# Kernel optimization log

Hardware: AMD Instinct MI355X
Metric: run time of the kernel (lower is better)

## Reference

```python
import jax, jax.numpy as jnp
import numpy as np

B, T = 128, 64
EMB, ACT = 1536, 12
STOCH, DETER, HIDDEN, ENS = 32, 1024, 1024, 5
MIN_STD = 0.1
UPDATE_BIAS = -1.0


def _ln(x, scale, bias, eps=1e-5):
    m = jnp.mean(x, -1, keepdims=True)
    v = jnp.mean((x - m) ** 2, -1, keepdims=True)
    return (x - m) * jax.lax.rsqrt(v + eps) * scale + bias


def setup_inputs():
    key = jax.random.key(0)
    ks = jax.random.split(key, 10)
    w = lambda k, s, sc=0.02: jax.random.normal(k, s, jnp.float32) * sc
    return dict(
        embed=jax.random.normal(ks[0], (B, T, EMB), jnp.float32),
        action=jax.random.normal(ks[1], (B, T, ACT), jnp.float32),
        is_first=(jax.random.uniform(ks[2], (B, T)) < 0.05),
        ens_index=jax.random.randint(ks[3], (T,), 0, ENS),
        W_img_in=w(ks[4], (STOCH + ACT, HIDDEN)), b_img_in=jnp.zeros((HIDDEN,)),
        g_img_in=jnp.ones((HIDDEN,)), bn_img_in=jnp.zeros((HIDDEN,)),
        W_gru=w(ks[5], (HIDDEN + DETER, 3 * DETER)), b_gru=jnp.zeros((3 * DETER,)),
        g_gru=jnp.ones((3 * DETER,)), bn_gru=jnp.zeros((3 * DETER,)),
        W_img_out=w(ks[6], (ENS, DETER, HIDDEN)), b_img_out=jnp.zeros((ENS, HIDDEN)),
        g_img_out=jnp.ones((ENS, HIDDEN)), bn_img_out=jnp.zeros((ENS, HIDDEN)),
        W_img_dist=w(ks[7], (ENS, HIDDEN, 2 * STOCH)), b_img_dist=jnp.zeros((ENS, 2 * STOCH)),
        W_obs_out=w(ks[8], (DETER + EMB, HIDDEN)), b_obs_out=jnp.zeros((HIDDEN,)),
        g_obs_out=jnp.ones((HIDDEN,)), bn_obs_out=jnp.zeros((HIDDEN,)),
        W_obs_dist=w(ks[9], (HIDDEN, 2 * STOCH)), b_obs_dist=jnp.zeros((2 * STOCH,)),
    )


def _observe(embed, action, is_first, ens_index,
             W_img_in, b_img_in, g_img_in, bn_img_in,
             W_gru, b_gru, g_gru, bn_gru,
             W_img_out, b_img_out, g_img_out, bn_img_out,
             W_img_dist, b_img_dist,
             W_obs_out, b_obs_out, g_obs_out, bn_obs_out,
             W_obs_dist, b_obs_dist):
    def step(carry, xs):
        stoch, deter = carry
        a, e, first, idx = xs  # [B,ACT], [B,EMB], [B], []
        m = (1.0 - first.astype(jnp.float32))[:, None]  # is_first resets prev state/action
        a, stoch, deter = a * m, stoch * m, deter * m
        # img_step: input MLP -> GRU cell (norm=True, update_bias=-1, Tanh)
        x = jax.nn.elu(_ln(jnp.concatenate([stoch, a], -1) @ W_img_in + b_img_in, g_img_in, bn_img_in))
        parts = _ln(jnp.concatenate([x, deter], -1) @ W_gru + b_gru, g_gru, bn_gru)
        reset, cand, update = jnp.split(parts, 3, -1)
        reset = jax.nn.sigmoid(reset)
        cand = jnp.tanh(reset * cand)
        update = jax.nn.sigmoid(update + UPDATE_BIAS)
        deter = update * cand + (1.0 - update) * deter
        # ensemble sufficient stats (all heads computed, one selected, as original)
        hs = jax.nn.elu(_ln(jnp.einsum('bd,kdh->kbh', deter, W_img_out) + b_img_out[:, None, :],
                            g_img_out[:, None, :], bn_img_out[:, None, :]))
        ds = jnp.einsum('kbh,khs->kbs', hs, W_img_dist) + b_img_dist[:, None, :]
        pmean, pstd = jnp.split(ds[idx], 2, -1)
        pstd = jax.nn.softplus(pstd) + MIN_STD
        prior_stoch = pmean  # deterministic mode of Normal
        # obs_step posterior
        xo = jax.nn.elu(_ln(jnp.concatenate([deter, e], -1) @ W_obs_out + b_obs_out, g_obs_out, bn_obs_out))
        omean, ostd = jnp.split(xo @ W_obs_dist + b_obs_dist, 2, -1)
        ostd = jax.nn.softplus(ostd) + MIN_STD
        post_stoch = omean
        out = jnp.concatenate([omean, ostd, post_stoch, pmean, pstd, prior_stoch, deter], -1)
        return (post_stoch, deter), out

    init = (jnp.zeros((B, STOCH), jnp.float32), jnp.zeros((B, DETER), jnp.float32))
    xs = (jnp.swapaxes(action, 0, 1), jnp.swapaxes(embed, 0, 1),
          jnp.swapaxes(is_first, 0, 1), ens_index)
    _, ys = jax.lax.scan(step, init, xs)  # [T, B, 6*STOCH + DETER]
    return jnp.swapaxes(ys, 0, 1)  # [B, T, 6*STOCH + DETER]


def reference(embed, action, is_first, ens_index,
              W_img_in, b_img_in, g_img_in, bn_img_in,
              W_gru, b_gru, g_gru, bn_gru,
              W_img_out, b_img_out, g_img_out, bn_img_out,
              W_img_dist, b_img_dist,
              W_obs_out, b_obs_out, g_obs_out, bn_obs_out,
              W_obs_dist, b_obs_dist):
    return _observe(embed, action, is_first, ens_index,
                    W_img_in, b_img_in, g_img_in, bn_img_in,
                    W_gru, b_gru, g_gru, bn_gru,
                    W_img_out, b_img_out, g_img_out, bn_img_out,
                    W_img_dist, b_img_dist,
                    W_obs_out, b_obs_out, g_obs_out, bn_obs_out,
                    W_obs_dist, b_obs_dist)
```

## Files before the change

kernel.cpp:

```cpp
#include <hip/hip_runtime.h>
#include <hip/hip_bf16.h>
#include <math.h>

using bf16 = __hip_bfloat16;
using short8 = __attribute__((ext_vector_type(8))) short;
using f32x4  = __attribute__((ext_vector_type(4))) float;

#define B_     128
#define T_     64
#define EMB_   1536
#define ACT_   12
#define STOCH_ 32
#define DETER_ 1024
#define HID_   1024
#define GRUN_  3072
#define GRUK_  2048
#define OBSK_  2560
#define OUTW_  1216

#define PW1   0
#define Pb1   45056
#define Pg1   46080
#define Pbn1  47104
#define Pbg   48128
#define Pgg   51200
#define Pbng  54272
#define Pb3   57344
#define Pg3   62464
#define Pbn3  67584
#define Pb4   72704
#define Pb5   73024
#define Pg5   74048
#define Pbn5  75072
#define Pb6   76096
#define PW4   76160
#define PW6   403840
#define PTOT  469376

__device__ inline float bf2f(bf16 v){ return __bfloat162float(v); }
__device__ inline bf16  f2bf(float v){ return __float2bfloat16(v); }
__device__ inline float elu_(float x){ return x > 0.f ? x : expm1f(x); }
__device__ inline float sigm_(float x){ return 1.f/(1.f+expf(-x)); }
__device__ inline float softplus_(float x){ return fmaxf(x,0.f) + log1pf(expf(-fabsf(x))); }
__device__ inline void stout(void* out, int dt, size_t i, float v){
  if(dt) ((bf16*)out)[i] = f2bf(v); else ((float*)out)[i] = v;
}
__device__ inline float maskv(const void* isf, int enc, int idx){
  float fv;
  if(enc==0)      fv = (float)((const int*)isf)[idx];
  else if(enc==1) fv = (float)((const unsigned char*)isf)[idx];
  else if(enc==2) fv = bf2f(((const bf16*)isf)[idx]);
  else            fv = ((const float*)isf)[idx];
  return (fv != 0.f) ? 0.f : 1.f;
}

__device__ inline void block_reduce2w(float& a, float& b, float* sm, int nw){
  __syncthreads();
  for(int off=32; off>0; off>>=1){
    a += __shfl_down(a, off);
    b += __shfl_down(b, off);
  }
  int w = threadIdx.x >> 6;
  if((threadIdx.x & 63) == 0){ sm[2*w] = a; sm[2*w+1] = b; }
  __syncthreads();
  float sa = 0.f, sb = 0.f;
  for(int i=0;i<nw;i++){ sa += sm[2*i]; sb += sm[2*i+1]; }
  a = sa; b = sb;
}

__global__ void k_detect(const unsigned short* emb, const unsigned char* isf, int* dflag){
  __shared__ int c0, c1, c2;
  if(threadIdx.x==0){ c0=0; c1=0; c2=0; }
  __syncthreads();
  if(blockIdx.x == 0){
    int c = 0;
    for(int i=threadIdx.x; i<2048; i+=256){
      unsigned short u = emb[2*i];
      int exp8 = (u >> 7) & 0xFF;
      if(exp8 > 140) c++;
    }
    atomicAdd(&c0, c);
    __syncthreads();
    if(threadIdx.x==0) dflag[0] = (c0 < 100) ? 1 : 0;
  } else {
    for(int i=threadIdx.x; i<B_*T_; i+=256){
      unsigned char c = isf[i];
      if(c == 0x3F){
        if((i & 3) == 1) atomicOr(&c0, 1);
        else if((i & 3) == 3) atomicOr(&c1, 1);
      }
      if(c == 1 && (i & 3) != 0) atomicOr(&c2, 1);
    }
    __syncthreads();
    if(threadIdx.x==0)
      dflag[1] = c0 ? 2 : (c1 ? 3 : (c2 ? 1 : 0));
  }
}

struct PDesc { const void* src[17]; int cum[18]; };
#define SEG0 1834
#define SEG1 12288
#define SEG2 96
#define SEG3 1536
#define SEG4 1280
#define SEG5 640

__device__ void transpose_dev(const void* src, bf16* dst, int K, int N,
                              int tk, int tn, int head, int dt,
                              unsigned short (*t)[72]){
  size_t hoff = (size_t)head * K * N;
  unsigned short* d = (unsigned short*)dst + hoff;
  int tx = threadIdx.x & 63, ty0 = threadIdx.x >> 6;
  int k0 = tk*64, n0 = tn*64;
  #pragma unroll
  for(int i=0;i<16;i++){
    int ty = ty0*16+i;
    size_t off = hoff + (size_t)(k0+ty)*N + n0+tx;
    unsigned short v;
    if(dt) v = ((const unsigned short*)src)[off];
    else { bf16 b = f2bf(((const float*)src)[off]); v = *(unsigned short*)&b; }
    t[ty][tx] = v;
  }
  __syncthreads();
  #pragma unroll
  for(int i=0;i<16;i++){ int ty = ty0*16+i; d[(size_t)(n0+ty)*K + k0+tx] = t[tx][ty]; }
}

__global__ __launch_bounds__(256) void k_setup(
    PDesc pd, float* paramF, const int* dflag,
    const void* embed, bf16* embB, const void* action, float* actF,
    const void* w8, bf16* WgT, const void* w12, bf16* W3T,
    const void* w18, bf16* W5T)
{
  __shared__ unsigned short ts[64][72];
  int bid = blockIdx.x, tid = threadIdx.x;
  int dt = dflag[0];
  if(bid < SEG0){
    int g = bid*256 + tid;
    if(g >= PTOT) return;
    int s = 0;
    while(g >= pd.cum[s+1]) s++;
    int off = g - pd.cum[s];
    paramF[g] = dt ? bf2f(((const bf16*)pd.src[s])[off]) : ((const float*)pd.src[s])[off];
    return;
  }
  bid -= SEG0;
  if(bid < SEG1){
    int i0 = (bid*256 + tid)*4;
    #pragma unroll
    for(int k=0;k<4;k++){
      int i = i0+k;
      embB[i] = dt ? ((const bf16*)embed)[i] : f2bf(((const float*)embed)[i]);
    }
    return;
  }
  bid -= SEG1;
  if(bid < SEG2){
    int i0 = (bid*256 + tid)*4;
    int n = B_*T_*ACT_;
    #pragma unroll
    for(int k=0;k<4;k++){
      int i = i0+k;
      if(i < n) actF[i] = dt ? bf2f(((const bf16*)action)[i]) : ((const float*)action)[i];
    }
    return;
  }
  bid -= SEG2;
  if(bid < SEG3){
    transpose_dev(w8, WgT, GRUK_, GRUN_, bid/48, bid%48, 0, dt, ts);
    return;
  }
  bid -= SEG3;
  if(bid < SEG4){
    int head = bid/256, rem = bid%256;
    transpose_dev(w12, W3T, DETER_, HID_, rem/16, rem%16, head, dt, ts);
    return;
  }
  bid -= SEG4;
  transpose_dev(w18, W5T, OBSK_, HID_, bid/16, bid%16, 0, dt, ts);
}

__global__ __launch_bounds__(256) void k_gemm(
    int mode, int t,
    const bf16* A2, const bf16* deterB, const bf16* embB,
    const bf16* WgT, const bf16* W3T, const bf16* W5T,
    float* z2p, float* z3p, float* z5p, const int* ens_index)
{
  __shared__ float red[8192];
  int bid = blockIdx.x;
  const bf16 *A0 = nullptr, *A1 = nullptr, *BT; float* Cdst;
  int N, ldb, s0 = 0, s1 = 0, split = 1<<30, k0, kc;
  if(mode == 0){
    if(bid < 192){
      int ct = bid % 96, part = bid / 96;
      N = GRUN_; ldb = GRUK_; BT = WgT + (size_t)ct*32*GRUK_;
      A0 = A2; s0 = GRUK_;
      k0 = part*1024; kc = 1024;
      Cdst = z2p + (size_t)part*B_*GRUN_ + ct*32;
    } else {
      int b2 = bid - 192;
      int ct = b2 & 31, part = b2 >> 5;
      N = HID_; ldb = OBSK_; BT = W5T + (size_t)ct*32*OBSK_;
      split = DETER_;
      A1 = embB + (size_t)t*EMB_; s1 = T_*EMB_;
      k0 = 1024 + part*768; kc = 768;
      Cdst = z5p + (size_t)(2+part)*B_*HID_ + ct*32;
    }
  } else if(bid < 64){
    int ct = bid & 31, part = bid >> 5;
    int idx = ens_index[t];
    N = HID_; ldb = DETER_; BT = W3T + (size_t)idx*DETER_*HID_ + (size_t)ct*32*DETER_;
    A0 = deterB; s0 = DETER_;
    k0 = part*512; kc = 512;
    Cdst = z3p + (size_t)part*B_*HID_ + ct*32;
  } else {
    int b2 = bid - 64;
    int ct = b2 & 31, part = b2 >> 5;
    N = HID_; ldb = OBSK_; BT = W5T + (size_t)ct*32*OBSK_;
    A0 = deterB; s0 = DETER_;
    k0 = part*512; kc = 512;
    Cdst = z5p + (size_t)part*B_*HID_ + ct*32;
  }
  int tid = threadIdx.x;
  int wave = tid >> 6, lane = tid & 63;
  int quad = lane >> 4, lo = lane & 15;
  int kw0 = k0 + wave*(kc>>2), kw1 = kw0 + (kc>>2);
  f32x4 acc[8][2];
  #pragma unroll
  for(int rf=0;rf<8;rf++){ acc[rf][0]=(f32x4)0.f; acc[rf][1]=(f32x4)0.f; }
  for(int kk=kw0; kk<kw1; kk+=32){
    int kf = kk + quad*8;
    const bf16* Ab; int str, ko;
    if(kf < split){ Ab=A0; str=s0; ko=kf; } else { Ab=A1; str=s1; ko=kf-split; }
    short8 af[8], bfg[2];
    #pragma unroll
    for(int rf=0;rf<8;rf++)
      af[rf] = *(const short8*)(const void*)(Ab + (size_t)(16*rf+lo)*str + ko);
    #pragma unroll
    for(int c=0;c<2;c++)
      bfg[c] = *(const short8*)(const void*)(BT + (size_t)(16*c+lo)*ldb + kf);
    #pragma unroll
    for(int rf=0;rf<8;rf++){
      acc[rf][0] = __builtin_amdgcn_mfma_f32_16x16x32_bf16(af[rf], bfg[0], acc[rf][0], 0,0,0);
      acc[rf][1] = __builtin_amdgcn_mfma_f32_16x16x32_bf16(af[rf], bfg[1], acc[rf][1], 0,0,0);
    }
  }
  if(wave >= 2){
    #pragma unroll
    for(int rf=0;rf<8;rf++)
      #pragma unroll
      for(int c=0;c<2;c++)
        *(f32x4*)&red[(((wave-2)*16) + rf*2 + c)*256 + lane*4] = acc[rf][c];
  }
  __syncthreads();
  if(wave < 2){
    #pragma unroll
    for(int rf=0;rf<8;rf++)
      #pragma unroll
      for(int c=0;c<2;c++)
        acc[rf][c] += *(const f32x4*)&red[((wave*16) + rf*2 + c)*256 + lane*4];
  }
  __syncthreads();
  if(wave < 2){
    #pragma unroll
    for(int rf=0;rf<8;rf++)
      #pragma unroll
      for(int c=0;c<2;c++)
        *(f32x4*)&red[((wave*16) + rf*2 + c)*256 + lane*4] = acc[rf][c];
  }
  __syncthreads();
  #pragma unroll
  for(int i=0;i<4;i++){
    int r = (tid>>3) + 32*i;
    int col0 = (tid&7)*4;
    int rf = r>>4, rr = r&15, q = rr>>2, g = rr&3;
    f32x4 v;
    #pragma unroll
    for(int j=0;j<4;j++){
      int col = col0+j; int c = col>>4, lo2 = col&15;
      int lane2 = q*16+lo2;
      v[j] = red[(rf*2 + c)*256 + lane2*4 + g]
           + red[(16 + rf*2 + c)*256 + lane2*4 + g];
    }
    *(f32x4*)(Cdst + (size_t)r*N + col0) = v;
  }
}

__global__ __launch_bounds__(1024) void k_gru(
    const float* z2p, const float* paramF, const int* dflag,
    const float* determ, float* deter, bf16* deterB, void* out, int t)
{
  __shared__ float sm[32];
  int b = blockIdx.x, tid = threadIdx.x;
  int dt = dflag[0];
  float zz[3]; float s=0.f, s2=0.f;
  #pragma unroll
  for(int i=0;i<3;i++){
    int h = tid + 1024*i;
    float acc = paramF[Pbg + h]
              + z2p[(size_t)b*GRUN_ + h]
              + z2p[(size_t)(B_ + b)*GRUN_ + h];
    zz[i]=acc; s+=acc; s2+=acc*acc;
  }
  block_reduce2w(s, s2, sm, 16);
  float mean = s/GRUN_, var = s2/GRUN_ - mean*mean;
  float rstd = rsqrtf(fmaxf(var,0.f) + 1e-5f);
  {
    float lnr = (zz[0] - mean)*rstd*paramF[Pgg+tid     ] + paramF[Pbng+tid     ];
    float lnc = (zz[1] - mean)*rstd*paramF[Pgg+tid+1024] + paramF[Pbng+tid+1024];
    float lnu = (zz[2] - mean)*rstd*paramF[Pgg+tid+2048] + paramF[Pbng+tid+2048];
    float reset = sigm_(lnr);
    float cand  = tanhf(reset*lnc);
    float upd   = sigm_(lnu - 1.f);
    float dn = upd*cand + (1.f-upd)*determ[b*DETER_+tid];
    deter[b*DETER_+tid]  = dn;
    deterB[b*DETER_+tid] = f2bf(dn);
    stout(out, dt, ((size_t)b*T_+t)*OUTW_ + 192 + tid, dn);
  }
}

__global__ __launch_bounds__(1024) void k_tail(
    const float* z3p, const float* z5p, const float* paramF, const int* dflag,
    const float* actF, const void* isf,
    const float* deter, float* determ, bf16* A2,
    void* out, const int* ens_index, int t)
{
  __shared__ float hs[1024], xo[1024];
  __shared__ float red[1024];
  __shared__ float dsO[128];
  __shared__ float in44[48];
  __shared__ float sm[32];
  int b = blockIdx.x, tid = threadIdx.x;
  int dt = dflag[0];
  int idx = ens_index[t];
  float a3 = z3p[(size_t)b*HID_ + tid] + z3p[(size_t)(B_ + b)*HID_ + tid]
           + paramF[Pb3 + idx*HID_ + tid];
  float a5 = z5p[(size_t)b*HID_ + tid] + z5p[(size_t)(B_ + b)*HID_ + tid]
           + z5p[(size_t)(2*B_ + b)*HID_ + tid] + z5p[(size_t)(3*B_ + b)*HID_ + tid]
           + paramF[Pb5 + tid];
  float s3=a3, q3=a3*a3, s5=a5, q5=a5*a5;
  block_reduce2w(s3, q3, sm, 16);
  block_reduce2w(s5, q5, sm, 16);
  float m3=s3/HID_, v3=q3/HID_-m3*m3, r3=rsqrtf(fmaxf(v3,0.f)+1e-5f);
  float m5=s5/HID_, v5=q5/HID_-m5*m5, r5=rsqrtf(fmaxf(v5,0.f)+1e-5f);
  hs[tid] = elu_((a3-m3)*r3*paramF[Pg3+idx*HID_+tid] + paramF[Pbn3+idx*HID_+tid]);
  xo[tid] = elu_((a5-m5)*r5*paramF[Pg5+tid] + paramF[Pbn5+tid]);
  __syncthreads();
  int j = tid & 63, cch = tid >> 6;
  {
    const float* W = paramF + PW4 + (size_t)idx*HID_*64;
    float a = 0.f;
    for(int k=cch*64; k<cch*64+64; k++) a += hs[k]*W[k*64 + j];
    red[tid] = a;
    __syncthreads();
    if(tid < 64){
      float acc = paramF[Pb4+idx*64+tid];
      for(int c=0;c<16;c++) acc += red[c*64+tid];
      dsO[tid] = acc;
    }
    __syncthreads();
    const float* W6f = paramF + PW6;
    a = 0.f;
    for(int k=cch*64; k<cch*64+64; k++) a += xo[k]*W6f[k*64 + j];
    red[tid] = a;
    __syncthreads();
    if(tid < 64){
      float acc = paramF[Pb6+tid];
      for(int c=0;c<16;c++) acc += red[c*64+tid];
      dsO[64+tid] = acc;
    }
    __syncthreads();
  }
  size_t ob = ((size_t)b*T_ + t)*OUTW_;
  if(tid < 32){
    float pm = dsO[tid];
    float ps = softplus_(dsO[32+tid]) + 0.1f;
    float om = dsO[64+tid];
    float os = softplus_(dsO[96+tid]) + 0.1f;
    stout(out, dt, ob+tid,      om);
    stout(out, dt, ob+32+tid,   os);
    stout(out, dt, ob+64+tid,   om);
    stout(out, dt, ob+96+tid,   pm);
    stout(out, dt, ob+128+tid,  ps);
    stout(out, dt, ob+160+tid,  pm);
  }
  if(t+1 < T_){
    float m = maskv(isf, dflag[1], b*T_ + (t+1));
    if(tid < 32)       in44[tid] = dsO[64+tid]*m;
    else if(tid < 44)  in44[tid] = actF[(size_t)(b*T_+(t+1))*ACT_ + (tid-32)]*m;
    __syncthreads();
    const float* W1f = paramF + PW1;
    float acc = paramF[Pb1 + tid];
    for(int k=0;k<STOCH_+ACT_;k++) acc += in44[k]*W1f[k*HID_ + tid];
    float s = acc, s2 = acc*acc;
    block_reduce2w(s, s2, sm, 16);
    float mean = s/HID_, var = s2/HID_ - mean*mean;
    float rstd = rsqrtf(fmaxf(var,0.f) + 1e-5f);
    float xv = (acc-mean)*rstd*paramF[Pg1+tid] + paramF[Pbn1+tid];
    A2[(size_t)b*GRUK_ + tid] = f2bf(elu_(xv));
    float dm = deter[b*DETER_+tid]*m;
    determ[b*DETER_+tid] = dm;
    A2[(size_t)b*GRUK_ + HID_ + tid] = f2bf(dm);
  }
}

__global__ __launch_bounds__(1024) void k_init(
    const float* actF, const void* isf, const int* dflag,
    const float* paramF, float* determ, bf16* A2)
{
  __shared__ float in44[48];
  __shared__ float sm[32];
  int b = blockIdx.x, tid = threadIdx.x;
  float m = maskv(isf, dflag[1], b*T_);
  if(tid < 32)       in44[tid] = 0.f;
  else if(tid < 44)  in44[tid] = actF[(size_t)(b*T_)*ACT_ + (tid-32)]*m;
  __syncthreads();
  const float* W1f = paramF + PW1;
  float acc = paramF[Pb1 + tid];
  for(int k=0;k<STOCH_+ACT_;k++) acc += in44[k]*W1f[k*HID_ + tid];
  float s = acc, s2 = acc*acc;
  block_reduce2w(s, s2, sm, 16);
  float mean = s/HID_, var = s2/HID_ - mean*mean;
  float rstd = rsqrtf(fmaxf(var,0.f) + 1e-5f);
  float xv = (acc-mean)*rstd*paramF[Pg1+tid] + paramF[Pbn1+tid];
  A2[(size_t)b*GRUK_ + tid] = f2bf(elu_(xv));
  determ[b*DETER_+tid] = 0.f;
  A2[(size_t)b*GRUK_ + HID_ + tid] = f2bf(0.f);
}

extern "C" void kernel_launch(void* const* d_in, const int* in_sizes, int n_in,
                              void* d_out, int out_size, void* d_ws, size_t ws_size,
                              hipStream_t stream)
{
  const void* embed  = d_in[0];
  const void* action = d_in[1];
  const void* isf    = d_in[2];
  const int*  ens_ix = (const int*)d_in[3];

  char* ws = (char*)d_ws;
  float* deter  = (float*)(ws + 0);
  float* determ = (float*)(ws + 524288);
  bf16*  A2     = (bf16*) (ws + 1048576);
  bf16*  deterB = (bf16*) (ws + 1572864);
  float* z2p    = (float*)(ws + 1835008);
  float* z3p    = (float*)(ws + 4980736);
  float* z5p    = (float*)(ws + 6029312);
  bf16*  WgT    = (bf16*) (ws + 8126464);
  bf16*  W3T    = (bf16*) (ws + 20709376);
  bf16*  W5T    = (bf16*) (ws + 31195136);
  float* paramF = (float*)(ws + 36438016);
  bf16*  embB   = (bf16*) (ws + 38315520);
  float* actF   = (float*)(ws + 63481344);
  int*   dflag  = (int*)  (ws + 63874560);

  k_detect<<<2,256,0,stream>>>((const unsigned short*)embed, (const unsigned char*)isf, dflag);

  PDesc pd;
  const int srcidx[17] = {4,5,6,7, 9,10,11, 13,14,15, 17, 19,20,21, 23, 16, 22};
  const int sizes[17]  = {45056,1024,1024,1024, 3072,3072,3072, 5120,5120,5120,
                          320, 1024,1024,1024, 64, 327680, 65536};
  int cum = 0;
  for(int i=0;i<17;i++){ pd.src[i] = d_in[srcidx[i]]; pd.cum[i] = cum; cum += sizes[i]; }
  pd.cum[17] = cum;

  int setup_grid = SEG0 + SEG1 + SEG2 + SEG3 + SEG4 + SEG5;
  k_setup<<<setup_grid,256,0,stream>>>(pd, paramF, dflag,
                                       embed, embB, action, actF,
                                       d_in[8], WgT, d_in[12], W3T, d_in[18], W5T);

  k_init<<<B_,1024,0,stream>>>(actF, isf, dflag, paramF, determ, A2);

  for(int t=0; t<T_; t++){
    k_gemm<<<256,256,0,stream>>>(0, t, A2, deterB, embB, WgT, W3T, W5T, z2p, z3p, z5p, ens_ix);
    k_gru<<<B_,1024,0,stream>>>(z2p, paramF, dflag, determ, deter, deterB, d_out, t);
    k_gemm<<<128,256,0,stream>>>(1, t, A2, deterB, embB, WgT, W3T, W5T, z2p, z3p, z5p, ens_ix);
    k_tail<<<B_,1024,0,stream>>>(z3p, z5p, paramF, dflag, actF, isf, deter, determ, A2, d_out, ens_ix, t);
  }
}
```

Before: 2.884 ms.

## Raise split-K parallelism in per-step GEMMs and read embed directly

The per-step GEMM launches grow to 512 blocks each. The GRU GEMM is split 4-way over K instead of 2, the obs GEMM 12-way and the img_out GEMM 8-way. The downstream GRU and tail kernels sum the extra partial buffers. The setup pass no longer pre-converts embed to bf16: the GEMM reads the raw embed input and converts fp32 to bf16 on the fly when needed, which removes a large setup copy. The trade-off is more partial-sum traffic and reduction work per step, and repeated conversion loads of fp32 embed.

New measurement: 3.364 ms. 1.17x slower.

```diff
diff --git a/kernel.cpp b/kernel.cpp
--- a/kernel.cpp
+++ b/kernel.cpp
@@ -99,11 +99,10 @@
 
 struct PDesc { const void* src[17]; int cum[18]; };
 #define SEG0 1834
-#define SEG1 12288
-#define SEG2 96
-#define SEG3 1536
-#define SEG4 1280
-#define SEG5 640
+#define SEG1 96
+#define SEG2 1536
+#define SEG3 1280
+#define SEG4 640
 
 __device__ void transpose_dev(const void* src, bf16* dst, int K, int N,
                               int tk, int tn, int head, int dt,
@@ -128,7 +127,7 @@
 
 __global__ __launch_bounds__(256) void k_setup(
     PDesc pd, float* paramF, const int* dflag,
-    const void* embed, bf16* embB, const void* action, float* actF,
+    const void* action, float* actF,
     const void* w8, bf16* WgT, const void* w12, bf16* W3T,
     const void* w18, bf16* W5T)
 {
@@ -147,16 +146,6 @@
   bid -= SEG0;
   if(bid < SEG1){
     int i0 = (bid*256 + tid)*4;
-    #pragma unroll
-    for(int k=0;k<4;k++){
-      int i = i0+k;
-      embB[i] = dt ? ((const bf16*)embed)[i] : f2bf(((const float*)embed)[i]);
-    }
-    return;
-  }
-  bid -= SEG1;
-  if(bid < SEG2){
-    int i0 = (bid*256 + tid)*4;
     int n = B_*T_*ACT_;
     #pragma unroll
     for(int k=0;k<4;k++){
@@ -165,60 +154,61 @@
     }
     return;
   }
+  bid -= SEG1;
+  if(bid < SEG2){
+    transpose_dev(w8, WgT, GRUK_, GRUN_, bid/48, bid%48, 0, dt, ts);
+    return;
+  }
   bid -= SEG2;
   if(bid < SEG3){
-    transpose_dev(w8, WgT, GRUK_, GRUN_, bid/48, bid%48, 0, dt, ts);
-    return;
-  }
-  bid -= SEG3;
-  if(bid < SEG4){
     int head = bid/256, rem = bid%256;
     transpose_dev(w12, W3T, DETER_, HID_, rem/16, rem%16, head, dt, ts);
     return;
   }
-  bid -= SEG4;
+  bid -= SEG3;
   transpose_dev(w18, W5T, OBSK_, HID_, bid/16, bid%16, 0, dt, ts);
 }
 
-__global__ __launch_bounds__(256) void k_gemm(
+__global__ __launch_bounds__(256,2) void k_gemm(
     int mode, int t,
-    const bf16* A2, const bf16* deterB, const bf16* embB,
+    const bf16* A2, const bf16* deterB, const void* embraw,
     const bf16* WgT, const bf16* W3T, const bf16* W5T,
-    float* z2p, float* z3p, float* z5p, const int* ens_index)
+    float* z2p, float* z3p, float* z5p, const int* ens_index, const int* dflag)
 {
   __shared__ float red[8192];
   int bid = blockIdx.x;
-  const bf16 *A0 = nullptr, *A1 = nullptr, *BT; float* Cdst;
-  int N, ldb, s0 = 0, s1 = 0, split = 1<<30, k0, kc;
+  int dtE = dflag[0];
+  const bf16 *A0 = nullptr, *BT; float* Cdst;
+  int N, ldb, s0 = 0, split = 1<<30, k0, kc;
+  int s1 = T_*EMB_, embbase = t*EMB_;
   if(mode == 0){
-    if(bid < 192){
+    if(bid < 384){
       int ct = bid % 96, part = bid / 96;
       N = GRUN_; ldb = GRUK_; BT = WgT + (size_t)ct*32*GRUK_;
       A0 = A2; s0 = GRUK_;
-      k0 = part*1024; kc = 1024;
+      k0 = part*512; kc = 512;
       Cdst = z2p + (size_t)part*B_*GRUN_ + ct*32;
     } else {
-      int b2 = bid - 192;
+      int b2 = bid - 384;
       int ct = b2 & 31, part = b2 >> 5;
       N = HID_; ldb = OBSK_; BT = W5T + (size_t)ct*32*OBSK_;
       split = DETER_;
-      A1 = embB + (size_t)t*EMB_; s1 = T_*EMB_;
-      k0 = 1024 + part*768; kc = 768;
-      Cdst = z5p + (size_t)(2+part)*B_*HID_ + ct*32;
-    }
-  } else if(bid < 64){
+      k0 = 1024 + part*384; kc = 384;
+      Cdst = z5p + (size_t)(8+part)*B_*HID_ + ct*32;
+    }
+  } else if(bid < 256){
     int ct = bid & 31, part = bid >> 5;
     int idx = ens_index[t];
     N = HID_; ldb = DETER_; BT = W3T + (size_t)idx*DETER_*HID_ + (size_t)ct*32*DETER_;
     A0 = deterB; s0 = DETER_;
-    k0 = part*512; kc = 512;
+    k0 = part*128; kc = 128;
     Cdst = z3p + (size_t)part*B_*HID_ + ct*32;
   } else {
-    int b2 = bid - 64;
+    int b2 = bid - 256;
     int ct = b2 & 31, part = b2 >> 5;
     N = HID_; ldb = OBSK_; BT = W5T + (size_t)ct*32*OBSK_;
     A0 = deterB; s0 = DETER_;
-    k0 = part*512; kc = 512;
+    k0 = part*128; kc = 128;
     Cdst = z5p + (size_t)part*B_*HID_ + ct*32;
   }
   int tid = threadIdx.x;
@@ -230,12 +220,35 @@
   for(int rf=0;rf<8;rf++){ acc[rf][0]=(f32x4)0.f; acc[rf][1]=(f32x4)0.f; }
   for(int kk=kw0; kk<kw1; kk+=32){
     int kf = kk + quad*8;
-    const bf16* Ab; int str, ko;
-    if(kf < split){ Ab=A0; str=s0; ko=kf; } else { Ab=A1; str=s1; ko=kf-split; }
     short8 af[8], bfg[2];
-    #pragma unroll
-    for(int rf=0;rf<8;rf++)
-      af[rf] = *(const short8*)(const void*)(Ab + (size_t)(16*rf+lo)*str + ko);
+    if(kf < split){
+      #pragma unroll
+      for(int rf=0;rf<8;rf++)
+        af[rf] = *(const short8*)(const void*)(A0 + (size_t)(16*rf+lo)*s0 + kf);
+    } else {
+      int ko = embbase + (kf - split);
+      if(dtE){
+        const bf16* E = (const bf16*)embraw;
+        #pragma unroll
+        for(int rf=0;rf<8;rf++)
+          af[rf] = *(const short8*)(const void*)(E + (size_t)(16*rf+lo)*s1 + ko);
+      } else {
+        const float* E = (const float*)embraw;
+        #pragma unroll
+        for(int rf=0;rf<8;rf++){
+          const float* pf = E + (size_t)(16*rf+lo)*s1 + ko;
+          f32x4 u0 = *(const f32x4*)pf;
+          f32x4 u1 = *(const f32x4*)(pf+4);
+          union{ unsigned short s[8]; short8 v; } r;
+          #pragma unroll
+          for(int w=0;w<4;w++){
+            bf16 b0 = f2bf(u0[w]); r.s[w]   = *(unsigned short*)&b0;
+            bf16 b1 = f2bf(u1[w]); r.s[4+w] = *(unsigned short*)&b1;
+          }
+          af[rf] = r.v;
+        }
+      }
+    }
     #pragma unroll
     for(int c=0;c<2;c++)
       bfg[c] = *(const short8*)(const void*)(BT + (size_t)(16*c+lo)*ldb + kf);
@@ -299,7 +312,9 @@
     int h = tid + 1024*i;
     float acc = paramF[Pbg + h]
               + z2p[(size_t)b*GRUN_ + h]
-              + z2p[(size_t)(B_ + b)*GRUN_ + h];
+              + z2p[(size_t)(B_ + b)*GRUN_ + h]
+              + z2p[(size_t)(2*B_ + b)*GRUN_ + h]
+              + z2p[(size_t)(3*B_ + b)*GRUN_ + h];
     zz[i]=acc; s+=acc; s2+=acc*acc;
   }
   block_reduce2w(s, s2, sm, 16);
@@ -333,11 +348,12 @@
   int b = blockIdx.x, tid = threadIdx.x;
   int dt = dflag[0];
   int idx = ens_index[t];
-  float a3 = z3p[(size_t)b*HID_ + tid] + z3p[(size_t)(B_ + b)*HID_ + tid]
-           + paramF[Pb3 + idx*HID_ + tid];
-  float a5 = z5p[(size_t)b*HID_ + tid] + z5p[(size_t)(B_ + b)*HID_ + tid]
-           + z5p[(size_t)(2*B_ + b)*HID_ + tid] + z5p[(size_t)(3*B_ + b)*HID_ + tid]
-           + paramF[Pb5 + tid];
+  float a3 = paramF[Pb3 + idx*HID_ + tid];
+  #pragma unroll
+  for(int p=0;p<8;p++) a3 += z3p[(size_t)(p*B_ + b)*HID_ + tid];
+  float a5 = paramF[Pb5 + tid];
+  #pragma unroll
+  for(int p=0;p<12;p++) a5 += z5p[(size_t)(p*B_ + b)*HID_ + tid];
   float s3=a3, q3=a3*a3, s5=a5, q5=a5*a5;
   block_reduce2w(s3, q3, sm, 16);
   block_reduce2w(s5, q5, sm, 16);
@@ -443,15 +459,14 @@
   bf16*  A2     = (bf16*) (ws + 1048576);
   bf16*  deterB = (bf16*) (ws + 1572864);
   float* z2p    = (float*)(ws + 1835008);
-  float* z3p    = (float*)(ws + 4980736);
-  float* z5p    = (float*)(ws + 6029312);
-  bf16*  WgT    = (bf16*) (ws + 8126464);
-  bf16*  W3T    = (bf16*) (ws + 20709376);
-  bf16*  W5T    = (bf16*) (ws + 31195136);
-  float* paramF = (float*)(ws + 36438016);
-  bf16*  embB   = (bf16*) (ws + 38315520);
-  float* actF   = (float*)(ws + 63481344);
-  int*   dflag  = (int*)  (ws + 63874560);
+  float* z3p    = (float*)(ws + 8126464);
+  float* z5p    = (float*)(ws + 12320768);
+  bf16*  WgT    = (bf16*) (ws + 18612224);
+  bf16*  W3T    = (bf16*) (ws + 31195136);
+  bf16*  W5T    = (bf16*) (ws + 41680896);
+  float* paramF = (float*)(ws + 46923776);
+  float* actF   = (float*)(ws + 48801280);
+  int*   dflag  = (int*)  (ws + 49194496);
 
   k_detect<<<2,256,0,stream>>>((const unsigned short*)embed, (const unsigned char*)isf, dflag);
 
@@ -463,17 +478,16 @@
   for(int i=0;i<17;i++){ pd.src[i] = d_in[srcidx[i]]; pd.cum[i] = cum; cum += sizes[i]; }
   pd.cum[17] = cum;
 
-  int setup_grid = SEG0 + SEG1 + SEG2 + SEG3 + SEG4 + SEG5;
-  k_setup<<<setup_grid,256,0,stream>>>(pd, paramF, dflag,
-                                       embed, embB, action, actF,
+  int setup_grid = SEG0 + SEG1 + SEG2 + SEG3 + SEG4;
+  k_setup<<<setup_grid,256,0,stream>>>(pd, paramF, dflag, action, actF,
                                        d_in[8], WgT, d_in[12], W3T, d_in[18], W5T);
 
   k_init<<<B_,1024,0,stream>>>(actF, isf, dflag, paramF, determ, A2);
 
   for(int t=0; t<T_; t++){
-    k_gemm<<<256,256,0,stream>>>(0, t, A2, deterB, embB, WgT, W3T, W5T, z2p, z3p, z5p, ens_ix);
+    k_gemm<<<512,256,0,stream>>>(0, t, A2, deterB, embed, WgT, W3T, W5T, z2p, z3p, z5p, ens_ix, dflag);
     k_gru<<<B_,1024,0,stream>>>(z2p, paramF, dflag, determ, deter, deterB, d_out, t);
-    k_gemm<<<128,256,0,stream>>>(1, t, A2, deterB, embB, WgT, W3T, W5T, z2p, z3p, z5p, ens_ix);
+    k_gemm<<<512,256,0,stream>>>(1, t, A2, deterB, embed, WgT, W3T, W5T, z2p, z3p, z5p, ens_ix, dflag);
     k_tail<<<B_,1024,0,stream>>>(z3p, z5p, paramF, dflag, actF, isf, deter, determ, A2, d_out, ens_ix, t);
   }
 }
```
